# Optimization experiments

Measured on AMD Instinct MI355X. Metric: run time of the kernel, lower is better.

Reference implementation:

```python
import jax, jax.numpy as jnp
import numpy as np

S, D, DR = 131072, 512, 512

def setup_inputs() -> dict:
    key = jax.random.key(0)
    k1, k2, k3, k4, k5 = jax.random.split(key, 5)
    scale = 1.0 / np.sqrt(D)
    return {
        "att_vectors": jax.random.normal(k1, (S, D), dtype=jnp.float32),
        "ref_vector": jax.random.normal(k2, (1, DR), dtype=jnp.float32),
        "Wh": jax.random.normal(k3, (D, D), dtype=jnp.float32) * scale,
        "Wv": jax.random.normal(k4, (D, DR), dtype=jnp.float32) * scale,
        "Ws": jax.random.normal(k5, (1, D), dtype=jnp.float32) * scale,
    }

def reference(att_vectors, ref_vector, Wh, Wv, Ws):
    # h = tanh(att @ Wh^T + ref @ Wv^T)  -> [S, D] (ref broadcasts over S)
    h = jnp.tanh(att_vectors @ Wh.T + ref_vector @ Wv.T)
    # scores [S] -> softmax over sequence
    scores = (h @ Ws.T)[:, 0]
    w = jax.nn.softmax(scores)
    # fused weighted sum replacing the python loop: [D]
    return jnp.einsum("s,sd->d", w, att_vectors)
```

## Files before the change

### kernel.cpp

```cpp
#include <hip/hip_runtime.h>
#include <hip/hip_bf16.h>
#include <stdint.h>


#define D_DIM 512
#define BM 128

typedef __attribute__((ext_vector_type(8))) short short8;
typedef __attribute__((ext_vector_type(4))) float f32x4;

#define WS_BIAS 0
#define WS_OUT  512
#define WS_Z    1024
#define WS_MB   1025
#define BPK_FLOAT_OFF 2048

#define WAITV4 asm volatile("s_waitcnt vmcnt(4)" ::: "memory")
#define WAITV0 asm volatile("s_waitcnt vmcnt(0)" ::: "memory")

__device__ __forceinline__ uint32_t pack2(float a, float b) {
    union { __hip_bfloat162 h; uint32_t u; } cv;
    cv.h = __float22bfloat162_rn(make_float2(a, b));
    return cv.u;
}
__device__ __forceinline__ float bf2f(unsigned short b) {
    return __uint_as_float(((uint32_t)b) << 16);
}
__device__ __forceinline__ float fast_tanh(float x) {
    float a = fabsf(x);
    float e = __expf(2.0f * a);
    float t = 1.0f - 2.0f / (e + 1.0f);
    return copysignf(t, x);
}
template<int CTRL>
__device__ __forceinline__ float dpp_add(float v) {
    int i = __builtin_amdgcn_mov_dpp(__float_as_int(v), CTRL, 0xf, 0xf, true);
    return v + __int_as_float(i);
}
__device__ __forceinline__ float reduce16(float v) {
    v = dpp_add<0xB1>(v);
    v = dpp_add<0x4E>(v);
    v = dpp_add<0x141>(v);
    v = dpp_add<0x140>(v);
    return v;
}
__device__ __forceinline__ void gl_lds16(const unsigned short* g, unsigned short* l) {
    __builtin_amdgcn_global_load_lds(
        (const __attribute__((address_space(1))) void*)g,
        (__attribute__((address_space(3))) void*)l, 16, 0, 0);
}

__global__ void k0_prep(const float* __restrict__ ref, const float* __restrict__ Wv,
                        const float* __restrict__ Ws, float* __restrict__ wsb) {
    __shared__ float red[256];
    const int tid = threadIdx.x;
    const int w = tid >> 6, l = tid & 63;
    const int d = blockIdx.x * 4 + w;
    const f32x4* rp = (const f32x4*)ref;
    const f32x4* vp = (const f32x4*)(Wv + (size_t)d * D_DIM);
    f32x4 r0 = rp[2 * l], r1 = rp[2 * l + 1];
    f32x4 v0 = vp[2 * l], v1 = vp[2 * l + 1];
    float acc = r0[0]*v0[0] + r0[1]*v0[1] + r0[2]*v0[2] + r0[3]*v0[3]
              + r1[0]*v1[0] + r1[1]*v1[1] + r1[2]*v1[2] + r1[3]*v1[3];
    #pragma unroll
    for (int m = 1; m < 64; m <<= 1) acc += __shfl_xor(acc, m, 64);
    if (l == 0) wsb[WS_BIAS + d] = acc;

    if (blockIdx.x == 0) {
        wsb[WS_OUT + tid] = 0.0f;
        wsb[WS_OUT + 256 + tid] = 0.0f;
        if (tid == 0) wsb[WS_Z] = 0.0f;
        red[tid] = fabsf(Ws[tid]) + fabsf(Ws[tid + 256]);
        __syncthreads();
        for (int off = 128; off > 0; off >>= 1) {
            if (tid < off) red[tid] += red[tid + off];
            __syncthreads();
        }
        if (tid == 0) wsb[WS_MB] = red[0];
    }
}

__global__ void kB_pack(const float* __restrict__ Wh, unsigned short* __restrict__ bpk) {
    const int t = blockIdx.x;
    const int g = t >> 4, kc = t & 15;
    #pragma unroll
    for (int h = 0; h < 2; ++h) {
        const int c = threadIdx.x + 256 * h;
        const int q = c >> 7, ns = (c >> 4) & 7, l15 = c & 15;
        const int n = g * 128 + ns * 16 + l15;
        const int k0 = kc * 32 + q * 8;
        const f32x4* wp = (const f32x4*)(Wh + (size_t)n * D_DIM + k0);
        f32x4 x0 = wp[0], x1 = wp[1];
        union { short8 s; uint32_t u[4]; } pk;
        pk.u[0] = pack2(x0[0], x0[1]);
        pk.u[1] = pack2(x0[2], x0[3]);
        pk.u[2] = pack2(x1[0], x1[1]);
        pk.u[3] = pack2(x1[2], x1[3]);
        *(short8*)(bpk + (size_t)t * 4096 + (size_t)c * 8) = pk.s;
    }
}

__launch_bounds__(256, 2)
__global__ void k1_main(const float* __restrict__ att,
                        const float* __restrict__ Ws,
                        const unsigned short* __restrict__ bpk, float* __restrict__ wsb) {
    __shared__ __align__(16) unsigned short Bt[6][4096];
    __shared__ float bias_s[512];
    __shared__ float wss_s[512];
    __shared__ float e_s[BM];
    __shared__ float out_s[512];

    const int tid = threadIdx.x;
    const int w   = tid >> 6;
    const int l   = tid & 63;
    const int l15 = l & 15;
    const int q   = l >> 4;
    const int row0 = blockIdx.x * BM;

    const unsigned short* bpk_w = bpk + (size_t)w * 1024 + (size_t)l * 8;

    #pragma unroll
    for (int t = 0; t < 2; ++t) {
        const unsigned short* s = bpk_w + (size_t)t * 4096;
        gl_lds16(s, &Bt[t][w * 1024]);
        gl_lds16(s + 512, &Bt[t][w * 1024 + 512]);
    }

    for (int i = tid; i < 512; i += 256) {
        bias_s[i] = wsb[WS_BIAS + i];
        wss_s[i]  = Ws[i];
        out_s[i]  = 0.0f;
    }
    const float mb = wsb[WS_MB];

    short8 afrag[2][16];
    #pragma unroll
    for (int t = 0; t < 2; ++t) {
        const int row = row0 + 32 * w + 16 * t + l15;
        const f32x4* ap = (const f32x4*)(att + (size_t)row * D_DIM + q * 8);
        #pragma unroll
        for (int kh = 0; kh < 2; ++kh) {
            #pragma unroll
            for (int kc8 = 0; kc8 < 8; ++kc8) {
                const int kc = kh * 8 + kc8;
                f32x4 x0 = ap[kc * 8];
                f32x4 x1 = ap[kc * 8 + 1];
                union { short8 s; uint32_t u[4]; } af;
                af.u[0] = pack2(x0[0], x0[1]);
                af.u[1] = pack2(x0[2], x0[3]);
                af.u[2] = pack2(x1[0], x1[1]);
                af.u[3] = pack2(x1[2], x1[3]);
                afrag[t][kc] = af.s;
            }
            __builtin_amdgcn_sched_barrier(0);
        }
    }

    #pragma unroll
    for (int t = 2; t < 4; ++t) {
        const unsigned short* s = bpk_w + (size_t)t * 4096;
        gl_lds16(s, &Bt[t][w * 1024]);
        gl_lds16(s + 512, &Bt[t][w * 1024 + 512]);
    }

    f32x4 acc[2][8];
    #pragma unroll
    for (int t = 0; t < 2; ++t)
        #pragma unroll
        for (int n = 0; n < 8; ++n) acc[t][n] = (f32x4){0.f, 0.f, 0.f, 0.f};
    float sc[8] = {0.f, 0.f, 0.f, 0.f, 0.f, 0.f, 0.f, 0.f};

    int bcur = 0;
    for (int g = 0; g < 4; ++g) {
        #pragma unroll
        for (int kp = 0; kp < 8; ++kp) {
            if (g == 3 && kp == 7) WAITV0; else WAITV4;
            __builtin_amdgcn_sched_barrier(0);
            __builtin_amdgcn_s_barrier();
            __builtin_amdgcn_sched_barrier(0);
            {
                const int tn = g * 16 + kp * 2 + 4;
                if (tn < 64) {
                    const int bpre = (bcur + 4 == 6) ? 0 : ((bcur + 4 == 8) ? 2 : 4);
                    #pragma unroll
                    for (int i = 0; i < 2; ++i) {
                        const unsigned short* s = bpk_w + (size_t)(tn + i) * 4096;
                        unsigned short* dld = &Bt[bpre + i][w * 1024];
                        gl_lds16(s, dld);
                        gl_lds16(s + 512, dld + 512);
                    }
                }
            }
            __builtin_amdgcn_s_setprio(1);
            #pragma unroll
            for (int i = 0; i < 2; ++i) {
                const unsigned short* bb = &Bt[0][0] + (size_t)(bcur + i) * 4096;
                #pragma unroll
                for (int ns = 0; ns < 8; ++ns) {
                    short8 bfr = *(const short8*)(bb + (q * 128 + ns * 16 + l15) * 8);
                    acc[0][ns] = __builtin_amdgcn_mfma_f32_16x16x32_bf16(afrag[0][kp * 2 + i], bfr, acc[0][ns], 0, 0, 0);
                    acc[1][ns] = __builtin_amdgcn_mfma_f32_16x16x32_bf16(afrag[1][kp * 2 + i], bfr, acc[1][ns], 0, 0, 0);
                }
            }
            __builtin_amdgcn_s_setprio(0);
            bcur = (bcur + 2 == 6) ? 0 : bcur + 2;
        }
        #pragma unroll
        for (int t = 0; t < 2; ++t) {
            #pragma unroll
            for (int ns = 0; ns < 8; ++ns) {
                const int c = g * 128 + ns * 16 + l15;
                const float bc = bias_s[c];
                const float wc = wss_s[c];
                f32x4 a = acc[t][ns];
                #pragma unroll
                for (int r = 0; r < 4; ++r)
                    sc[t * 4 + r] += fast_tanh(a[r] + bc) * wc;
                acc[t][ns] = (f32x4){0.f, 0.f, 0.f, 0.f};
            }
        }
    }

    #pragma unroll
    for (int i = 0; i < 8; ++i) sc[i] = reduce16(sc[i]);

    if (l15 == 0) {
        #pragma unroll
        for (int t = 0; t < 2; ++t)
            #pragma unroll
            for (int r = 0; r < 4; ++r)
                e_s[32 * w + 16 * t + q * 4 + r] = __expf(sc[t * 4 + r] - mb);
    }
    __syncthreads();

    if (w == 0) {
        float z = e_s[l] + e_s[l + 64];
        #pragma unroll
        for (int m = 1; m < 64; m <<= 1) z += __shfl_xor(z, m, 64);
        if (l == 0) atomicAdd(&wsb[WS_Z], z);
    }

    const float el0 = e_s[32 * w + l15];
    const float el1 = e_s[32 * w + 16 + l15];
    #pragma unroll
    for (int kc = 0; kc < 16; ++kc) {
        float o[8];
        #pragma unroll
        for (int j = 0; j < 8; ++j) {
            o[j] = el0 * bf2f((unsigned short)afrag[0][kc][j])
                 + el1 * bf2f((unsigned short)afrag[1][kc][j]);
            o[j] = reduce16(o[j]);
        }
        if (l15 == 0) {
            #pragma unroll
            for (int j = 0; j < 8; ++j)
                atomicAdd(&out_s[kc * 32 + q * 8 + j], o[j]);
        }
    }
    __syncthreads();
    for (int i = tid; i < 512; i += 256)
        atomicAdd(&wsb[WS_OUT + i], out_s[i]);
}

__global__ void k2_fin(const float* __restrict__ wsb, float* __restrict__ out) {
    const float z = wsb[WS_Z];
    out[threadIdx.x] = wsb[WS_OUT + threadIdx.x] / z;
}

extern "C" void kernel_launch(void* const* d_in, const int* in_sizes, int n_in,
                              void* d_out, int out_size, void* d_ws, size_t ws_size,
                              hipStream_t stream) {
    const float* att = (const float*)d_in[0];
    const float* ref = (const float*)d_in[1];
    const float* Wh  = (const float*)d_in[2];
    const float* Wv  = (const float*)d_in[3];
    const float* Ws  = (const float*)d_in[4];
    float* out = (float*)d_out;
    float* wsb = (float*)d_ws;

    unsigned short* bpk = (unsigned short*)(wsb + BPK_FLOAT_OFF);

    hipLaunchKernelGGL(k0_prep, dim3(128), dim3(256), 0, stream, ref, Wv, Ws, wsb);
    hipLaunchKernelGGL(kB_pack, dim3(64), dim3(256), 0, stream, Wh, bpk);
    hipLaunchKernelGGL(k1_main, dim3(131072 / BM), dim3(256), 0, stream, att, Ws, bpk, wsb);
    hipLaunchKernelGGL(k2_fin, dim3(1), dim3(512), 0, stream, wsb, out);
}
```

Before: 467.9 us.

## Switch B-tile pipeline to ping-pong double buffer of four-tile phases

Replaces the six-slot rotating LDS ring, which fetched two tiles per step with a vmcnt(4) wait, by an eight-slot ping-pong buffer. Each phase prefetches four k-tiles while computing on the other four, with a full vmcnt(0) wait and one barrier per phase, which halves the number of barriers. LDS fragment reads are batched four at a time ahead of the MFMAs, with sched barriers in between. LDS use grows by 16 KB per block, which may reduce occupancy at two blocks per CU, and the full wait drains all outstanding loads each phase.

```diff
diff --git a/kernel.cpp b/kernel.cpp
--- a/kernel.cpp
+++ b/kernel.cpp
@@ -15,7 +15,6 @@
 #define WS_MB   1025
 #define BPK_FLOAT_OFF 2048
 
-#define WAITV4 asm volatile("s_waitcnt vmcnt(4)" ::: "memory")
 #define WAITV0 asm volatile("s_waitcnt vmcnt(0)" ::: "memory")
 
 __device__ __forceinline__ uint32_t pack2(float a, float b) {
@@ -104,7 +103,7 @@
 __global__ void k1_main(const float* __restrict__ att,
                         const float* __restrict__ Ws,
                         const unsigned short* __restrict__ bpk, float* __restrict__ wsb) {
-    __shared__ __align__(16) unsigned short Bt[6][4096];
+    __shared__ __align__(16) unsigned short Bt[8][4096];
     __shared__ float bias_s[512];
     __shared__ float wss_s[512];
     __shared__ float e_s[BM];
@@ -120,7 +119,7 @@
     const unsigned short* bpk_w = bpk + (size_t)w * 1024 + (size_t)l * 8;
 
     #pragma unroll
-    for (int t = 0; t < 2; ++t) {
+    for (int t = 0; t < 4; ++t) {
         const unsigned short* s = bpk_w + (size_t)t * 4096;
         gl_lds16(s, &Bt[t][w * 1024]);
         gl_lds16(s + 512, &Bt[t][w * 1024 + 512]);
@@ -156,13 +155,6 @@
         }
     }
 
-    #pragma unroll
-    for (int t = 2; t < 4; ++t) {
-        const unsigned short* s = bpk_w + (size_t)t * 4096;
-        gl_lds16(s, &Bt[t][w * 1024]);
-        gl_lds16(s + 512, &Bt[t][w * 1024 + 512]);
-    }
-
     f32x4 acc[2][8];
     #pragma unroll
     for (int t = 0; t < 2; ++t)
@@ -170,40 +162,50 @@
         for (int n = 0; n < 8; ++n) acc[t][n] = (f32x4){0.f, 0.f, 0.f, 0.f};
     float sc[8] = {0.f, 0.f, 0.f, 0.f, 0.f, 0.f, 0.f, 0.f};
 
-    int bcur = 0;
     for (int g = 0; g < 4; ++g) {
         #pragma unroll
-        for (int kp = 0; kp < 8; ++kp) {
-            if (g == 3 && kp == 7) WAITV0; else WAITV4;
+        for (int pq = 0; pq < 4; ++pq) {
+            WAITV0;
             __builtin_amdgcn_sched_barrier(0);
             __builtin_amdgcn_s_barrier();
             __builtin_amdgcn_sched_barrier(0);
             {
-                const int tn = g * 16 + kp * 2 + 4;
-                if (tn < 64) {
-                    const int bpre = (bcur + 4 == 6) ? 0 : ((bcur + 4 == 8) ? 2 : 4);
+                const int phn = g * 4 + pq + 1;
+                if (phn < 16) {
+                    const int bb = (phn & 1) * 4;
                     #pragma unroll
-                    for (int i = 0; i < 2; ++i) {
-                        const unsigned short* s = bpk_w + (size_t)(tn + i) * 4096;
-                        unsigned short* dld = &Bt[bpre + i][w * 1024];
+                    for (int i = 0; i < 4; ++i) {
+                        const unsigned short* s = bpk_w + (size_t)(phn * 4 + i) * 4096;
+                        unsigned short* dld = &Bt[bb + i][w * 1024];
                         gl_lds16(s, dld);
                         gl_lds16(s + 512, dld + 512);
                     }
                 }
             }
             __builtin_amdgcn_s_setprio(1);
-            #pragma unroll
-            for (int i = 0; i < 2; ++i) {
-                const unsigned short* bb = &Bt[0][0] + (size_t)(bcur + i) * 4096;
+            const int bq = (pq & 1) * 4;
+            #pragma unroll
+            for (int i = 0; i < 4; ++i) {
+                const int kc = pq * 4 + i;
+                const unsigned short* bb2 = &Bt[bq + i][0];
                 #pragma unroll
-                for (int ns = 0; ns < 8; ++ns) {
-                    short8 bfr = *(const short8*)(bb + (q * 128 + ns * 16 + l15) * 8);
-                    acc[0][ns] = __builtin_amdgcn_mfma_f32_16x16x32_bf16(afrag[0][kp * 2 + i], bfr, acc[0][ns], 0, 0, 0);
-                    acc[1][ns] = __builtin_amdgcn_mfma_f32_16x16x32_bf16(afrag[1][kp * 2 + i], bfr, acc[1][ns], 0, 0, 0);
+                for (int h = 0; h < 2; ++h) {
+                    short8 bfr[4];
+                    #pragma unroll
+                    for (int n2 = 0; n2 < 4; ++n2) {
+                        const int ns = h * 4 + n2;
+                        bfr[n2] = *(const short8*)(bb2 + (q * 128 + ns * 16 + l15) * 8);
+                    }
+                    #pragma unroll
+                    for (int n2 = 0; n2 < 4; ++n2) {
+                        const int ns = h * 4 + n2;
+                        acc[0][ns] = __builtin_amdgcn_mfma_f32_16x16x32_bf16(afrag[0][kc], bfr[n2], acc[0][ns], 0, 0, 0);
+                        acc[1][ns] = __builtin_amdgcn_mfma_f32_16x16x32_bf16(afrag[1][kc], bfr[n2], acc[1][ns], 0, 0, 0);
+                    }
+                    __builtin_amdgcn_sched_barrier(0);
                 }
             }
             __builtin_amdgcn_s_setprio(0);
-            bcur = (bcur + 2 == 6) ? 0 : bcur + 2;
         }
         #pragma unroll
         for (int t = 0; t < 2; ++t) {
```

Result: no change. 459.3 us (-1.9%).
